# Performance work log

Hardware: AMD Instinct MI355X
Metric: run time of the kernel (lower is better)

The kernel has to match this reference:

```python
import jax, jax.numpy as jnp
import numpy as np

NHID = 1024
# Canonical DARTS recurrent genotype: (activation, predecessor-state index)
GENOTYPE = [("sigmoid", 0), ("relu", 1), ("relu", 1), ("identity", 1),
            ("tanh", 2), ("sigmoid", 5), ("tanh", 3), ("relu", 5)]
CONCAT = [1, 2, 3, 4, 5, 6, 7, 8]

_ACTS = {"tanh": jnp.tanh, "relu": jax.nn.relu,
         "sigmoid": jax.nn.sigmoid, "identity": lambda z: z}


def _cell(x, h_prev, W0, Ws):
    # x: [B, ninp], h_prev: [B, nhid]
    xh = jnp.concatenate([x, h_prev], axis=-1)              # [B, ninp+nhid]
    c0, h0 = jnp.split(xh @ W0, 2, axis=-1)                 # each [B, nhid]
    s0 = h_prev + jax.nn.sigmoid(c0) * (jnp.tanh(h0) - h_prev)
    states = [s0]
    for i, (name, pred) in enumerate(GENOTYPE):
        s_prev = states[pred]
        c, h = jnp.split(s_prev @ Ws[i], 2, axis=-1)
        s = s_prev + jax.nn.sigmoid(c) * (_ACTS[name](h) - s_prev)
        states.append(s)
    return jnp.mean(jnp.stack([states[i] for i in CONCAT], axis=-1), axis=-1)


def setup_inputs() -> dict:
    key = jax.random.key(0)
    k1, k2, k3 = jax.random.split(key, 3)
    T, B, NINP = 256, 256, 1024
    inputs = jax.random.normal(k1, (T, B, NINP), dtype=jnp.float32)
    h0 = jnp.zeros((B, NHID), dtype=jnp.float32)
    W0 = jax.random.normal(k2, (NINP + NHID, 2 * NHID), dtype=jnp.float32) * 0.02
    Ws = jax.random.normal(k3, (len(GENOTYPE), NHID, 2 * NHID), dtype=jnp.float32) * 0.02
    return {"inputs": inputs, "h0": h0, "W0": W0, "Ws": Ws}


def reference(inputs, h0, W0, Ws):
    def step(h, x):
        h_new = _cell(x, h, W0, Ws)
        return h_new, h_new
    _, hiddens = jax.lax.scan(step, h0, inputs)             # [T, B, nhid]
    return hiddens
```

## Files before the change

kernel.cpp:

```cpp
#include <hip/hip_runtime.h>


typedef short short8 __attribute__((ext_vector_type(8)));
typedef float floatx4 __attribute__((ext_vector_type(4)));

#define MFMA __builtin_amdgcn_mfma_f32_16x16x32_bf16

enum { ACT_SIG = 0, ACT_RELU = 1, ACT_TANH = 2, ACT_ID = 3 };

__device__ __forceinline__ unsigned short f2bf(float f) {
  unsigned u = __builtin_bit_cast(unsigned, f);
  u += 0x7fffu + ((u >> 16) & 1u);
  return (unsigned short)(u >> 16);
}

__device__ __forceinline__ float sigf(float z) { return 1.f / (1.f + __expf(-z)); }

__device__ __forceinline__ float actf(int a, float h) {
  if (a == ACT_SIG)  return sigf(h);
  if (a == ACT_RELU) return fmaxf(h, 0.f);
  if (a == ACT_TANH) return 1.f - 2.f / (__expf(2.f * h) + 1.f);
  return h;
}


struct GJob {
  const unsigned short* A;
  const unsigned short* Wt;
  const float* base;
  float* out_f;
  unsigned short* out_b;
  int act;
  int K;
};
struct GJobs { GJob j[3]; };

struct Set6 { short8 a0, a1, b0, b1, b2, b3; };

__device__ __forceinline__ void load6(Set6& s,
    const unsigned short* pa0, const unsigned short* pa1,
    const unsigned short* pb0, const unsigned short* pb1,
    const unsigned short* pb2, const unsigned short* pb3, int k) {
  s.a0 = *(const short8*)(pa0 + k);
  s.a1 = *(const short8*)(pa1 + k);
  s.b0 = *(const short8*)(pb0 + k);
  s.b1 = *(const short8*)(pb1 + k);
  s.b2 = *(const short8*)(pb2 + k);
  s.b3 = *(const short8*)(pb3 + k);
}

__device__ __forceinline__ void mm6(const Set6& s, floatx4 ac[2][2], floatx4 ah[2][2]) {
  ac[0][0] = MFMA(s.a0, s.b0, ac[0][0], 0, 0, 0);
  ac[1][0] = MFMA(s.a1, s.b0, ac[1][0], 0, 0, 0);
  ac[0][1] = MFMA(s.a0, s.b1, ac[0][1], 0, 0, 0);
  ac[1][1] = MFMA(s.a1, s.b1, ac[1][1], 0, 0, 0);
  ah[0][0] = MFMA(s.a0, s.b2, ah[0][0], 0, 0, 0);
  ah[1][0] = MFMA(s.a1, s.b2, ah[1][0], 0, 0, 0);
  ah[0][1] = MFMA(s.a0, s.b3, ah[0][1], 0, 0, 0);
  ah[1][1] = MFMA(s.a1, s.b3, ah[1][1], 0, 0, 0);
}

__global__ __launch_bounds__(256) void phase_gemm(GJobs jobs) {
  const GJob jb = jobs.j[blockIdx.z];
  const int K = jb.K;
  const int lane = threadIdx.x & 63;
  const int wave = threadIdx.x >> 6;
  const int col = lane & 15, quad = lane >> 4;
  const int m0  = blockIdx.y * 64 + (wave >> 1) * 32;
  const int sc0 = blockIdx.x * 64 + (wave & 1) * 32;

  const unsigned short* pa0 = jb.A + (size_t)(m0 + col) * K + quad * 8;
  const unsigned short* pa1 = pa0 + (size_t)16 * K;
  const unsigned short* pb0 = jb.Wt + (size_t)(sc0 + col) * K + quad * 8;
  const unsigned short* pb1 = pb0 + (size_t)16 * K;
  const unsigned short* pb2 = jb.Wt + (size_t)(1024 + sc0 + col) * K + quad * 8;
  const unsigned short* pb3 = pb2 + (size_t)16 * K;

  floatx4 ac[2][2], ah[2][2];
#pragma unroll
  for (int i = 0; i < 2; ++i)
#pragma unroll
    for (int j = 0; j < 2; ++j) {
      ac[i][j] = (floatx4){0.f, 0.f, 0.f, 0.f};
      ah[i][j] = (floatx4){0.f, 0.f, 0.f, 0.f};
    }

  Set6 s0, s1;
  load6(s0, pa0, pa1, pb0, pb1, pb2, pb3, 0);
  load6(s1, pa0, pa1, pb0, pb1, pb2, pb3, 32);
  for (int k = 64; k < K; k += 64) {
    mm6(s0, ac, ah);
    load6(s0, pa0, pa1, pb0, pb1, pb2, pb3, k);
    mm6(s1, ac, ah);
    load6(s1, pa0, pa1, pb0, pb1, pb2, pb3, k + 32);
  }
  mm6(s0, ac, ah);
  mm6(s1, ac, ah);

  const int act = jb.act;
#pragma unroll
  for (int mi = 0; mi < 2; ++mi)
#pragma unroll
    for (int ni = 0; ni < 2; ++ni)
#pragma unroll
      for (int rr = 0; rr < 4; ++rr) {
        int m = m0 + mi * 16 + quad * 4 + rr;
        int n = sc0 + ni * 16 + col;
        int idx = m * 1024 + n;
        float c = ac[mi][ni][rr];
        float h = ah[mi][ni][rr];
        float p = jb.base[idx];
        float v = fmaf(sigf(c), actf(act, h) - p, p);
        jb.out_f[idx] = v;
        if (jb.out_b) jb.out_b[idx] = f2bf(v);
      }
}

struct Set10 { short8 a0, a1, u0, u1, u2, u3, v0, v1, v2, v3; };

__global__ __launch_bounds__(256) void phase_e(
    const unsigned short* __restrict__ A,
    const unsigned short* __restrict__ W5t,
    const unsigned short* __restrict__ W7t,
    const float* __restrict__ m1, const float* __restrict__ m2,
    const float* __restrict__ m3, const float* __restrict__ m4,
    const float* __restrict__ m5, const float* __restrict__ m7,
    const float* __restrict__ xnext,
    float* __restrict__ out_t,
    unsigned short* __restrict__ xhb) {
  const int lane = threadIdx.x & 63;
  const int wave = threadIdx.x >> 6;
  const int col = lane & 15, quad = lane >> 4;
  const int m0  = blockIdx.y * 64 + (wave >> 1) * 32;
  const int sc0 = blockIdx.x * 64 + (wave & 1) * 32;
  const int K = 1024;

  const unsigned short* pa0 = A + (size_t)(m0 + col) * K + quad * 8;
  const unsigned short* pa1 = pa0 + (size_t)16 * K;
  const unsigned short* pu0 = W5t + (size_t)(sc0 + col) * K + quad * 8;
  const unsigned short* pu1 = pu0 + (size_t)16 * K;
  const unsigned short* pu2 = W5t + (size_t)(1024 + sc0 + col) * K + quad * 8;
  const unsigned short* pu3 = pu2 + (size_t)16 * K;
  const unsigned short* pv0 = W7t + (size_t)(sc0 + col) * K + quad * 8;
  const unsigned short* pv1 = pv0 + (size_t)16 * K;
  const unsigned short* pv2 = W7t + (size_t)(1024 + sc0 + col) * K + quad * 8;
  const unsigned short* pv3 = pv2 + (size_t)16 * K;

  floatx4 acc[4][2][2];
#pragma unroll
  for (int w = 0; w < 4; ++w)
#pragma unroll
    for (int i = 0; i < 2; ++i)
#pragma unroll
      for (int j = 0; j < 2; ++j) acc[w][i][j] = (floatx4){0.f, 0.f, 0.f, 0.f};

  Set10 s0, s1;
#define LOAD10(s, k)                                     \
  do {                                                   \
    s.a0 = *(const short8*)(pa0 + (k));                  \
    s.a1 = *(const short8*)(pa1 + (k));                  \
    s.u0 = *(const short8*)(pu0 + (k));                  \
    s.u1 = *(const short8*)(pu1 + (k));                  \
    s.u2 = *(const short8*)(pu2 + (k));                  \
    s.u3 = *(const short8*)(pu3 + (k));                  \
    s.v0 = *(const short8*)(pv0 + (k));                  \
    s.v1 = *(const short8*)(pv1 + (k));                  \
    s.v2 = *(const short8*)(pv2 + (k));                  \
    s.v3 = *(const short8*)(pv3 + (k));                  \
  } while (0)
#define MM10(s)                                          \
  do {                                                   \
    acc[0][0][0] = MFMA(s.a0, s.u0, acc[0][0][0], 0,0,0);\
    acc[0][1][0] = MFMA(s.a1, s.u0, acc[0][1][0], 0,0,0);\
    acc[0][0][1] = MFMA(s.a0, s.u1, acc[0][0][1], 0,0,0);\
    acc[0][1][1] = MFMA(s.a1, s.u1, acc[0][1][1], 0,0,0);\
    acc[1][0][0] = MFMA(s.a0, s.u2, acc[1][0][0], 0,0,0);\
    acc[1][1][0] = MFMA(s.a1, s.u2, acc[1][1][0], 0,0,0);\
    acc[1][0][1] = MFMA(s.a0, s.u3, acc[1][0][1], 0,0,0);\
    acc[1][1][1] = MFMA(s.a1, s.u3, acc[1][1][1], 0,0,0);\
    acc[2][0][0] = MFMA(s.a0, s.v0, acc[2][0][0], 0,0,0);\
    acc[2][1][0] = MFMA(s.a1, s.v0, acc[2][1][0], 0,0,0);\
    acc[2][0][1] = MFMA(s.a0, s.v1, acc[2][0][1], 0,0,0);\
    acc[2][1][1] = MFMA(s.a1, s.v1, acc[2][1][1], 0,0,0);\
    acc[3][0][0] = MFMA(s.a0, s.v2, acc[3][0][0], 0,0,0);\
    acc[3][1][0] = MFMA(s.a1, s.v2, acc[3][1][0], 0,0,0);\
    acc[3][0][1] = MFMA(s.a0, s.v3, acc[3][0][1], 0,0,0);\
    acc[3][1][1] = MFMA(s.a1, s.v3, acc[3][1][1], 0,0,0);\
  } while (0)

  LOAD10(s0, 0);
  LOAD10(s1, 32);
  for (int k = 64; k < K; k += 64) {
    MM10(s0);
    LOAD10(s0, k);
    MM10(s1);
    LOAD10(s1, k + 32);
  }
  MM10(s0);
  MM10(s1);

#pragma unroll
  for (int mi = 0; mi < 2; ++mi)
#pragma unroll
    for (int ni = 0; ni < 2; ++ni)
#pragma unroll
      for (int rr = 0; rr < 4; ++rr) {
        int m = m0 + mi * 16 + quad * 4 + rr;
        int n = sc0 + ni * 16 + col;
        int idx = m * 1024 + n;
        float b = m5[idx];
        float s6 = fmaf(sigf(acc[0][mi][ni][rr]), sigf(acc[1][mi][ni][rr]) - b, b);
        float s8 = fmaf(sigf(acc[2][mi][ni][rr]), fmaxf(acc[3][mi][ni][rr], 0.f) - b, b);
        float sum = m1[idx] + m2[idx] + m3[idx] + m4[idx] + b + m7[idx] + s6 + s8;
        float hh = sum * 0.125f;
        out_t[idx] = hh;
        xhb[m * 2048 + 1024 + n] = f2bf(hh);
        xhb[m * 2048 + n] = f2bf(xnext[idx]);
      }
}

__global__ __launch_bounds__(256) void conv_w(const float* __restrict__ W0,
                                              const float* __restrict__ Wsrc,
                                              unsigned short* __restrict__ wt) {
  int job = blockIdx.z;
  int K = (job == 0) ? 2048 : 1024;
  int kt = blockIdx.y;
  if (kt * 32 >= K) return;
  int nt = blockIdx.x;
  const float* W = (job == 0) ? W0 : (Wsrc + (size_t)(job - 1) * 1024 * 2048);
  unsigned short* Wt = (job == 0) ? wt
      : (wt + (size_t)2048 * 2048 + (size_t)(job - 1) * 2048 * 1024);

  __shared__ unsigned short tile[32][33];
  int tx = threadIdx.x & 31;
  int ty = threadIdx.x >> 5;
#pragma unroll
  for (int i = 0; i < 4; ++i) {
    int k = kt * 32 + ty + i * 8;
    tile[ty + i * 8][tx] = f2bf(W[(size_t)k * 2048 + nt * 32 + tx]);
  }
  __syncthreads();
#pragma unroll
  for (int i = 0; i < 4; ++i) {
    int n = nt * 32 + ty + i * 8;
    Wt[(size_t)n * K + kt * 32 + tx] = tile[tx][ty + i * 8];
  }
}

__global__ __launch_bounds__(256) void init_xh(const float* __restrict__ x0,
                                               const float* __restrict__ h0,
                                               unsigned short* __restrict__ xhb) {
  int i = blockIdx.x * 256 + threadIdx.x;
  int m = i >> 10, n = i & 1023;
  xhb[m * 2048 + n] = f2bf(x0[i]);
  xhb[m * 2048 + 1024 + n] = f2bf(h0[i]);
}

extern "C" void kernel_launch(void* const* d_in, const int* in_sizes, int n_in,
                              void* d_out, int out_size, void* d_ws, size_t ws_size,
                              hipStream_t stream) {
  const float* x_all = (const float*)d_in[0];
  const float* h0    = (const float*)d_in[1];
  const float* W0    = (const float*)d_in[2];
  const float* Ws    = (const float*)d_in[3];
  float* out = (float*)d_out;

  const size_t BH = (size_t)256 * 1024;

  unsigned short* wt0 = (unsigned short*)d_ws;
  unsigned short* wts[8];
  for (int i = 0; i < 8; ++i)
    wts[i] = wt0 + (size_t)2048 * 2048 + (size_t)i * 2048 * 1024;
  float* smbase = (float*)((char*)d_ws +
      (size_t)(2048 * 2048 + 8 * 2048 * 1024) * 2);
  float* sm[7];
  for (int i = 0; i < 7; ++i) sm[i] = smbase + (size_t)i * BH;
  unsigned short* sbbase = (unsigned short*)(smbase + (size_t)7 * BH);
  unsigned short* sb[5];
  for (int i = 0; i < 5; ++i) sb[i] = sbbase + (size_t)i * BH;
  unsigned short* xhb = sbbase + (size_t)5 * BH;

  conv_w<<<dim3(64, 64, 9), 256, 0, stream>>>(W0, Ws, wt0);
  init_xh<<<dim3(1024), 256, 0, stream>>>(x_all, h0, xhb);

  for (int t = 0; t < 256; ++t) {
    const float* hp = (t == 0) ? h0 : (out + (size_t)(t - 1) * BH);
    float* o_t = out + (size_t)t * BH;
    const float* xnext = x_all + (size_t)((t < 255) ? t + 1 : 255) * BH;

    GJobs J{};
    J.j[0] = { xhb, wt0, hp, sm[0], sb[0], ACT_TANH, 2048 };
    phase_gemm<<<dim3(16, 4, 1), 256, 0, stream>>>(J);

    J = GJobs{};
    J.j[0] = { sb[0], wts[0], sm[0], sm[1], sb[1], ACT_SIG, 1024 };
    phase_gemm<<<dim3(16, 4, 1), 256, 0, stream>>>(J);

    J = GJobs{};
    J.j[0] = { sb[1], wts[1], sm[1], sm[2], sb[2], ACT_RELU, 1024 };
    J.j[1] = { sb[1], wts[2], sm[1], sm[3], sb[3], ACT_RELU, 1024 };
    phase_gemm<<<dim3(16, 4, 2), 256, 0, stream>>>(J);

    J = GJobs{};
    J.j[0] = { sb[2], wts[4], sm[2], sm[5], sb[4], ACT_TANH, 1024 };
    J.j[1] = { sb[3], wts[6], sm[3], sm[6], nullptr, ACT_TANH, 1024 };
    J.j[2] = { sb[1], wts[3], sm[1], sm[4], nullptr, ACT_ID, 1024 };
    phase_gemm<<<dim3(16, 4, 3), 256, 0, stream>>>(J);

    phase_e<<<dim3(16, 4, 1), 256, 0, stream>>>(
        sb[4], wts[5], wts[7],
        sm[1], sm[2], sm[3], sm[4], sm[5], sm[6],
        xnext, o_t, xhb);
  }
}
```

Baseline: 44.52 ms.

## Replace per-step kernel launches with a persistent kernel using grid barriers

Replaces the 1280 small per-phase kernel launches with one persistent 256-block kernel that loops over timesteps and separates phases with an atomic-counter grid barrier. Tiles are made smaller (32x16 or 32x32 per wave) so 256 blocks, rather than 64-192, share each phase, and prefetch depth becomes a template parameter. The aim is to remove launch overhead and raise occupancy across CUs. In exchange it relies on every block being co-resident, and the spin barrier gives up after a timeout, which could silently yield wrong results.

```diff
diff --git a/kernel.cpp b/kernel.cpp
--- a/kernel.cpp
+++ b/kernel.cpp
@@ -23,200 +23,260 @@
   return h;
 }
 
-
-struct GJob {
-  const unsigned short* A;
-  const unsigned short* Wt;
-  const float* base;
-  float* out_f;
-  unsigned short* out_b;
-  int act;
-  int K;
-};
-struct GJobs { GJob j[3]; };
-
-struct Set6 { short8 a0, a1, b0, b1, b2, b3; };
-
-__device__ __forceinline__ void load6(Set6& s,
-    const unsigned short* pa0, const unsigned short* pa1,
-    const unsigned short* pb0, const unsigned short* pb1,
-    const unsigned short* pb2, const unsigned short* pb3, int k) {
-  s.a0 = *(const short8*)(pa0 + k);
-  s.a1 = *(const short8*)(pa1 + k);
-  s.b0 = *(const short8*)(pb0 + k);
-  s.b1 = *(const short8*)(pb1 + k);
-  s.b2 = *(const short8*)(pb2 + k);
-  s.b3 = *(const short8*)(pb3 + k);
-}
-
-__device__ __forceinline__ void mm6(const Set6& s, floatx4 ac[2][2], floatx4 ah[2][2]) {
-  ac[0][0] = MFMA(s.a0, s.b0, ac[0][0], 0, 0, 0);
-  ac[1][0] = MFMA(s.a1, s.b0, ac[1][0], 0, 0, 0);
-  ac[0][1] = MFMA(s.a0, s.b1, ac[0][1], 0, 0, 0);
-  ac[1][1] = MFMA(s.a1, s.b1, ac[1][1], 0, 0, 0);
-  ah[0][0] = MFMA(s.a0, s.b2, ah[0][0], 0, 0, 0);
-  ah[1][0] = MFMA(s.a1, s.b2, ah[1][0], 0, 0, 0);
-  ah[0][1] = MFMA(s.a0, s.b3, ah[0][1], 0, 0, 0);
-  ah[1][1] = MFMA(s.a1, s.b3, ah[1][1], 0, 0, 0);
-}
-
-__global__ __launch_bounds__(256) void phase_gemm(GJobs jobs) {
-  const GJob jb = jobs.j[blockIdx.z];
-  const int K = jb.K;
-  const int lane = threadIdx.x & 63;
-  const int wave = threadIdx.x >> 6;
+__device__ __forceinline__ bool grid_sync(unsigned* bar, unsigned target,
+                                          bool skip_wait) {
+  __shared__ int gs_flag;
+  __syncthreads();
+  if (threadIdx.x == 0) {
+    __hip_atomic_fetch_add(bar, 1u, __ATOMIC_RELEASE, __HIP_MEMORY_SCOPE_AGENT);
+    int ok = 1;
+    if (!skip_wait) {
+      int spins = 0;
+      while (__hip_atomic_load(bar, __ATOMIC_RELAXED,
+                               __HIP_MEMORY_SCOPE_AGENT) < target) {
+        __builtin_amdgcn_s_sleep(16);
+        if (++spins > (1 << 19)) { ok = 0; break; }
+      }
+    }
+    gs_flag = ok;
+  }
+  __syncthreads();
+  __builtin_amdgcn_fence(__ATOMIC_ACQUIRE, "agent");
+  return gs_flag != 0;
+}
+
+template <int NB, int DEPTH>
+__device__ __forceinline__ void g2_tile(
+    const unsigned short* __restrict__ A, const unsigned short* __restrict__ Wt,
+    const float* __restrict__ base, float* __restrict__ out_f,
+    unsigned short* __restrict__ out_b, int act, int K, int m0, int sc0,
+    int lane) {
   const int col = lane & 15, quad = lane >> 4;
-  const int m0  = blockIdx.y * 64 + (wave >> 1) * 32;
-  const int sc0 = blockIdx.x * 64 + (wave & 1) * 32;
-
-  const unsigned short* pa0 = jb.A + (size_t)(m0 + col) * K + quad * 8;
+  const unsigned short* pa0 = A + (size_t)(m0 + col) * K + quad * 8;
   const unsigned short* pa1 = pa0 + (size_t)16 * K;
-  const unsigned short* pb0 = jb.Wt + (size_t)(sc0 + col) * K + quad * 8;
-  const unsigned short* pb1 = pb0 + (size_t)16 * K;
-  const unsigned short* pb2 = jb.Wt + (size_t)(1024 + sc0 + col) * K + quad * 8;
-  const unsigned short* pb3 = pb2 + (size_t)16 * K;
-
-  floatx4 ac[2][2], ah[2][2];
+  const unsigned short* pbc[NB];
+  const unsigned short* pbh[NB];
+#pragma unroll
+  for (int j = 0; j < NB; ++j) {
+    pbc[j] = Wt + (size_t)(sc0 + 16 * j + col) * K + quad * 8;
+    pbh[j] = Wt + (size_t)(1024 + sc0 + 16 * j + col) * K + quad * 8;
+  }
+
+  floatx4 ac[2][NB], ah[2][NB];
 #pragma unroll
   for (int i = 0; i < 2; ++i)
 #pragma unroll
-    for (int j = 0; j < 2; ++j) {
+    for (int j = 0; j < NB; ++j) {
       ac[i][j] = (floatx4){0.f, 0.f, 0.f, 0.f};
       ah[i][j] = (floatx4){0.f, 0.f, 0.f, 0.f};
     }
 
-  Set6 s0, s1;
-  load6(s0, pa0, pa1, pb0, pb1, pb2, pb3, 0);
-  load6(s1, pa0, pa1, pb0, pb1, pb2, pb3, 32);
-  for (int k = 64; k < K; k += 64) {
-    mm6(s0, ac, ah);
-    load6(s0, pa0, pa1, pb0, pb1, pb2, pb3, k);
-    mm6(s1, ac, ah);
-    load6(s1, pa0, pa1, pb0, pb1, pb2, pb3, k + 32);
-  }
-  mm6(s0, ac, ah);
-  mm6(s1, ac, ah);
-
-  const int act = jb.act;
+  short8 ra0[DEPTH], ra1[DEPTH], rbc[DEPTH][NB], rbh[DEPTH][NB];
+
+#define G2_LD(s, k)                                                            \
+  {                                                                            \
+    ra0[s] = *(const short8*)(pa0 + (k));                                      \
+    ra1[s] = *(const short8*)(pa1 + (k));                                      \
+    _Pragma("unroll") for (int j = 0; j < NB; ++j) {                           \
+      rbc[s][j] = *(const short8*)(pbc[j] + (k));                              \
+      rbh[s][j] = *(const short8*)(pbh[j] + (k));                              \
+    }                                                                          \
+  }
+#define G2_MM(s)                                                               \
+  {                                                                            \
+    _Pragma("unroll") for (int j = 0; j < NB; ++j) {                           \
+      ac[0][j] = MFMA(ra0[s], rbc[s][j], ac[0][j], 0, 0, 0);                   \
+      ac[1][j] = MFMA(ra1[s], rbc[s][j], ac[1][j], 0, 0, 0);                   \
+      ah[0][j] = MFMA(ra0[s], rbh[s][j], ah[0][j], 0, 0, 0);                   \
+      ah[1][j] = MFMA(ra1[s], rbh[s][j], ah[1][j], 0, 0, 0);                   \
+    }                                                                          \
+  }
+
+#pragma unroll
+  for (int s = 0; s < DEPTH; ++s) G2_LD(s, s * 32);
+  for (int k = DEPTH * 32; k < K; k += DEPTH * 32) {
+#pragma unroll
+    for (int s = 0; s < DEPTH; ++s) {
+      G2_MM(s);
+      G2_LD(s, k + s * 32);
+    }
+  }
+#pragma unroll
+  for (int s = 0; s < DEPTH; ++s) G2_MM(s);
+#undef G2_LD
+#undef G2_MM
+
 #pragma unroll
   for (int mi = 0; mi < 2; ++mi)
 #pragma unroll
-    for (int ni = 0; ni < 2; ++ni)
+    for (int j = 0; j < NB; ++j)
 #pragma unroll
       for (int rr = 0; rr < 4; ++rr) {
         int m = m0 + mi * 16 + quad * 4 + rr;
-        int n = sc0 + ni * 16 + col;
+        int n = sc0 + j * 16 + col;
         int idx = m * 1024 + n;
-        float c = ac[mi][ni][rr];
-        float h = ah[mi][ni][rr];
-        float p = jb.base[idx];
+        float c = ac[mi][j][rr];
+        float h = ah[mi][j][rr];
+        float p = base[idx];
         float v = fmaf(sigf(c), actf(act, h) - p, p);
-        jb.out_f[idx] = v;
-        if (jb.out_b) jb.out_b[idx] = f2bf(v);
+        out_f[idx] = v;
+        if (out_b) out_b[idx] = f2bf(v);
       }
 }
 
-struct Set10 { short8 a0, a1, u0, u1, u2, u3, v0, v1, v2, v3; };
-
-__global__ __launch_bounds__(256) void phase_e(
-    const unsigned short* __restrict__ A,
-    const unsigned short* __restrict__ W5t,
-    const unsigned short* __restrict__ W7t,
-    const float* __restrict__ m1, const float* __restrict__ m2,
-    const float* __restrict__ m3, const float* __restrict__ m4,
-    const float* __restrict__ m5, const float* __restrict__ m7,
-    const float* __restrict__ xnext,
-    float* __restrict__ out_t,
-    unsigned short* __restrict__ xhb) {
-  const int lane = threadIdx.x & 63;
-  const int wave = threadIdx.x >> 6;
+__device__ __forceinline__ void e_tile(
+    const unsigned short* __restrict__ A, const unsigned short* __restrict__ W5t,
+    const unsigned short* __restrict__ W7t, const float* __restrict__ m1,
+    const float* __restrict__ m2, const float* __restrict__ m3,
+    const float* __restrict__ m4, const float* __restrict__ m5,
+    const float* __restrict__ m7, const float* __restrict__ xnext,
+    float* __restrict__ out_t, unsigned short* __restrict__ xhb,
+    int m0, int sc0, int lane) {
   const int col = lane & 15, quad = lane >> 4;
-  const int m0  = blockIdx.y * 64 + (wave >> 1) * 32;
-  const int sc0 = blockIdx.x * 64 + (wave & 1) * 32;
   const int K = 1024;
-
   const unsigned short* pa0 = A + (size_t)(m0 + col) * K + quad * 8;
   const unsigned short* pa1 = pa0 + (size_t)16 * K;
   const unsigned short* pu0 = W5t + (size_t)(sc0 + col) * K + quad * 8;
-  const unsigned short* pu1 = pu0 + (size_t)16 * K;
-  const unsigned short* pu2 = W5t + (size_t)(1024 + sc0 + col) * K + quad * 8;
-  const unsigned short* pu3 = pu2 + (size_t)16 * K;
+  const unsigned short* pu1 = W5t + (size_t)(1024 + sc0 + col) * K + quad * 8;
   const unsigned short* pv0 = W7t + (size_t)(sc0 + col) * K + quad * 8;
-  const unsigned short* pv1 = pv0 + (size_t)16 * K;
-  const unsigned short* pv2 = W7t + (size_t)(1024 + sc0 + col) * K + quad * 8;
-  const unsigned short* pv3 = pv2 + (size_t)16 * K;
-
-  floatx4 acc[4][2][2];
-#pragma unroll
-  for (int w = 0; w < 4; ++w)
-#pragma unroll
-    for (int i = 0; i < 2; ++i)
-#pragma unroll
-      for (int j = 0; j < 2; ++j) acc[w][i][j] = (floatx4){0.f, 0.f, 0.f, 0.f};
-
-  Set10 s0, s1;
-#define LOAD10(s, k)                                     \
-  do {                                                   \
-    s.a0 = *(const short8*)(pa0 + (k));                  \
-    s.a1 = *(const short8*)(pa1 + (k));                  \
-    s.u0 = *(const short8*)(pu0 + (k));                  \
-    s.u1 = *(const short8*)(pu1 + (k));                  \
-    s.u2 = *(const short8*)(pu2 + (k));                  \
-    s.u3 = *(const short8*)(pu3 + (k));                  \
-    s.v0 = *(const short8*)(pv0 + (k));                  \
-    s.v1 = *(const short8*)(pv1 + (k));                  \
-    s.v2 = *(const short8*)(pv2 + (k));                  \
-    s.v3 = *(const short8*)(pv3 + (k));                  \
-  } while (0)
-#define MM10(s)                                          \
-  do {                                                   \
-    acc[0][0][0] = MFMA(s.a0, s.u0, acc[0][0][0], 0,0,0);\
-    acc[0][1][0] = MFMA(s.a1, s.u0, acc[0][1][0], 0,0,0);\
-    acc[0][0][1] = MFMA(s.a0, s.u1, acc[0][0][1], 0,0,0);\
-    acc[0][1][1] = MFMA(s.a1, s.u1, acc[0][1][1], 0,0,0);\
-    acc[1][0][0] = MFMA(s.a0, s.u2, acc[1][0][0], 0,0,0);\
-    acc[1][1][0] = MFMA(s.a1, s.u2, acc[1][1][0], 0,0,0);\
-    acc[1][0][1] = MFMA(s.a0, s.u3, acc[1][0][1], 0,0,0);\
-    acc[1][1][1] = MFMA(s.a1, s.u3, acc[1][1][1], 0,0,0);\
-    acc[2][0][0] = MFMA(s.a0, s.v0, acc[2][0][0], 0,0,0);\
-    acc[2][1][0] = MFMA(s.a1, s.v0, acc[2][1][0], 0,0,0);\
-    acc[2][0][1] = MFMA(s.a0, s.v1, acc[2][0][1], 0,0,0);\
-    acc[2][1][1] = MFMA(s.a1, s.v1, acc[2][1][1], 0,0,0);\
-    acc[3][0][0] = MFMA(s.a0, s.v2, acc[3][0][0], 0,0,0);\
-    acc[3][1][0] = MFMA(s.a1, s.v2, acc[3][1][0], 0,0,0);\
-    acc[3][0][1] = MFMA(s.a0, s.v3, acc[3][0][1], 0,0,0);\
-    acc[3][1][1] = MFMA(s.a1, s.v3, acc[3][1][1], 0,0,0);\
-  } while (0)
-
-  LOAD10(s0, 0);
-  LOAD10(s1, 32);
+  const unsigned short* pv1 = W7t + (size_t)(1024 + sc0 + col) * K + quad * 8;
+
+  floatx4 c6[2], h6[2], c8[2], h8[2];
+#pragma unroll
+  for (int i = 0; i < 2; ++i) {
+    c6[i] = (floatx4){0.f, 0.f, 0.f, 0.f};
+    h6[i] = (floatx4){0.f, 0.f, 0.f, 0.f};
+    c8[i] = (floatx4){0.f, 0.f, 0.f, 0.f};
+    h8[i] = (floatx4){0.f, 0.f, 0.f, 0.f};
+  }
+
+  short8 ra0[2], ra1[2], ru0[2], ru1[2], rv0[2], rv1[2];
+#define E_LD(s, k)                              \
+  {                                             \
+    ra0[s] = *(const short8*)(pa0 + (k));       \
+    ra1[s] = *(const short8*)(pa1 + (k));       \
+    ru0[s] = *(const short8*)(pu0 + (k));       \
+    ru1[s] = *(const short8*)(pu1 + (k));       \
+    rv0[s] = *(const short8*)(pv0 + (k));       \
+    rv1[s] = *(const short8*)(pv1 + (k));       \
+  }
+#define E_MM(s)                                 \
+  {                                             \
+    c6[0] = MFMA(ra0[s], ru0[s], c6[0], 0, 0, 0); \
+    c6[1] = MFMA(ra1[s], ru0[s], c6[1], 0, 0, 0); \
+    h6[0] = MFMA(ra0[s], ru1[s], h6[0], 0, 0, 0); \
+    h6[1] = MFMA(ra1[s], ru1[s], h6[1], 0, 0, 0); \
+    c8[0] = MFMA(ra0[s], rv0[s], c8[0], 0, 0, 0); \
+    c8[1] = MFMA(ra1[s], rv0[s], c8[1], 0, 0, 0); \
+    h8[0] = MFMA(ra0[s], rv1[s], h8[0], 0, 0, 0); \
+    h8[1] = MFMA(ra1[s], rv1[s], h8[1], 0, 0, 0); \
+  }
+
+  E_LD(0, 0);
+  E_LD(1, 32);
   for (int k = 64; k < K; k += 64) {
-    MM10(s0);
-    LOAD10(s0, k);
-    MM10(s1);
-    LOAD10(s1, k + 32);
-  }
-  MM10(s0);
-  MM10(s1);
+    E_MM(0);
+    E_LD(0, k);
+    E_MM(1);
+    E_LD(1, k + 32);
+  }
+  E_MM(0);
+  E_MM(1);
+#undef E_LD
+#undef E_MM
 
 #pragma unroll
   for (int mi = 0; mi < 2; ++mi)
 #pragma unroll
-    for (int ni = 0; ni < 2; ++ni)
-#pragma unroll
-      for (int rr = 0; rr < 4; ++rr) {
-        int m = m0 + mi * 16 + quad * 4 + rr;
-        int n = sc0 + ni * 16 + col;
-        int idx = m * 1024 + n;
-        float b = m5[idx];
-        float s6 = fmaf(sigf(acc[0][mi][ni][rr]), sigf(acc[1][mi][ni][rr]) - b, b);
-        float s8 = fmaf(sigf(acc[2][mi][ni][rr]), fmaxf(acc[3][mi][ni][rr], 0.f) - b, b);
-        float sum = m1[idx] + m2[idx] + m3[idx] + m4[idx] + b + m7[idx] + s6 + s8;
-        float hh = sum * 0.125f;
-        out_t[idx] = hh;
-        xhb[m * 2048 + 1024 + n] = f2bf(hh);
-        xhb[m * 2048 + n] = f2bf(xnext[idx]);
-      }
+    for (int rr = 0; rr < 4; ++rr) {
+      int m = m0 + mi * 16 + quad * 4 + rr;
+      int n = sc0 + col;
+      int idx = m * 1024 + n;
+      float b = m5[idx];
+      float s6 = fmaf(sigf(c6[mi][rr]), sigf(h6[mi][rr]) - b, b);
+      float s8 = fmaf(sigf(c8[mi][rr]), fmaxf(h8[mi][rr], 0.f) - b, b);
+      float sum = m1[idx] + m2[idx] + m3[idx] + m4[idx] + b + m7[idx] + s6 + s8;
+      float hh = sum * 0.125f;
+      out_t[idx] = hh;
+      xhb[m * 2048 + 1024 + n] = f2bf(hh);
+      xhb[m * 2048 + n] = f2bf(xnext[idx]);
+    }
+}
+
+__global__ __launch_bounds__(512, 2) void darts_persist(
+    const float* __restrict__ x_all, const float* __restrict__ h0,
+    const unsigned short* __restrict__ wtb, float* out, float* __restrict__ smb,
+    unsigned short* __restrict__ sbb, unsigned short* __restrict__ xhb,
+    unsigned* __restrict__ bar) {
+  const size_t BH = (size_t)256 * 1024;
+  const int lane = threadIdx.x & 63;
+  const int wave = threadIdx.x >> 6;
+  const int blk = blockIdx.x;
+
+#define WTS(i) (wtb + (size_t)2048 * 2048 + (size_t)(i) * 2048 * 1024)
+  float* sm0 = smb;
+  float* sm1 = smb + 1 * BH;
+  float* sm2 = smb + 2 * BH;
+  float* sm3 = smb + 3 * BH;
+  float* sm4 = smb + 4 * BH;
+  float* sm5 = smb + 5 * BH;
+  float* sm6 = smb + 6 * BH;
+  unsigned short* sb0 = sbb;
+  unsigned short* sb1 = sbb + 1 * BH;
+  unsigned short* sb2 = sbb + 2 * BH;
+  unsigned short* sb3 = sbb + 3 * BH;
+  unsigned short* sb4 = sbb + 4 * BH;
+
+  bool poisoned = false;
+  unsigned tgt = 0;
+  for (int t = 0; t < 256; ++t) {
+    const float* hp = (t == 0) ? h0 : (out + (size_t)(t - 1) * BH);
+    float* o_t = out + (size_t)t * BH;
+    const float* xnext = x_all + (size_t)((t < 255) ? t + 1 : 255) * BH;
+
+    if (wave < 2) {
+      int tau = wave * 256 + blk;
+      g2_tile<1, 4>(xhb, wtb, hp, sm0, sb0, ACT_TANH, 2048,
+                    (tau >> 6) * 32, (tau & 63) * 16, lane);
+    }
+    tgt += 256; poisoned |= !grid_sync(bar, tgt, poisoned);
+
+    if (wave < 2) {
+      int tau = wave * 256 + blk;
+      g2_tile<1, 4>(sb0, WTS(0), sm0, sm1, sb1, ACT_SIG, 1024,
+                    (tau >> 6) * 32, (tau & 63) * 16, lane);
+    }
+    tgt += 256; poisoned |= !grid_sync(bar, tgt, poisoned);
+
+    if (wave < 3) {
+      const unsigned short* W = (wave == 0) ? WTS(1) : (wave == 1) ? WTS(2) : WTS(3);
+      float* of = (wave == 0) ? sm2 : (wave == 1) ? sm3 : sm4;
+      unsigned short* ob = (wave == 0) ? sb2 : (wave == 1) ? sb3 : (unsigned short*)nullptr;
+      int act = (wave == 2) ? ACT_ID : ACT_RELU;
+      g2_tile<2, 2>(sb1, W, sm1, of, ob, act, 1024,
+                    (blk >> 5) * 32, (blk & 31) * 32, lane);
+    }
+    tgt += 256; poisoned |= !grid_sync(bar, tgt, poisoned);
+
+    if (wave < 2) {
+      const unsigned short* Aop = (wave == 0) ? sb2 : sb3;
+      const unsigned short* W = (wave == 0) ? WTS(4) : WTS(6);
+      const float* bs = (wave == 0) ? sm2 : sm3;
+      float* of = (wave == 0) ? sm5 : sm6;
+      unsigned short* ob = (wave == 0) ? sb4 : (unsigned short*)nullptr;
+      g2_tile<2, 2>(Aop, W, bs, of, ob, ACT_TANH, 1024,
+                    (blk >> 5) * 32, (blk & 31) * 32, lane);
+    }
+    tgt += 256; poisoned |= !grid_sync(bar, tgt, poisoned);
+
+    if (wave < 2) {
+      int tau = wave * 256 + blk;
+      e_tile(sb4, WTS(5), WTS(7), sm1, sm2, sm3, sm4, sm5, sm6,
+             xnext, o_t, xhb, (tau >> 6) * 32, (tau & 63) * 16, lane);
+    }
+    tgt += 256; poisoned |= !grid_sync(bar, tgt, poisoned);
+  }
+#undef WTS
 }
 
 __global__ __launch_bounds__(256) void conv_w(const float* __restrict__ W0,
@@ -256,6 +316,8 @@
   xhb[m * 2048 + 1024 + n] = f2bf(h0[i]);
 }
 
+__global__ void zero_bar(unsigned* bar) { *bar = 0u; }
+
 extern "C" void kernel_launch(void* const* d_in, const int* in_sizes, int n_in,
                               void* d_out, int out_size, void* d_ws, size_t ws_size,
                               hipStream_t stream) {
@@ -268,48 +330,15 @@
   const size_t BH = (size_t)256 * 1024;
 
   unsigned short* wt0 = (unsigned short*)d_ws;
-  unsigned short* wts[8];
-  for (int i = 0; i < 8; ++i)
-    wts[i] = wt0 + (size_t)2048 * 2048 + (size_t)i * 2048 * 1024;
   float* smbase = (float*)((char*)d_ws +
       (size_t)(2048 * 2048 + 8 * 2048 * 1024) * 2);
-  float* sm[7];
-  for (int i = 0; i < 7; ++i) sm[i] = smbase + (size_t)i * BH;
   unsigned short* sbbase = (unsigned short*)(smbase + (size_t)7 * BH);
-  unsigned short* sb[5];
-  for (int i = 0; i < 5; ++i) sb[i] = sbbase + (size_t)i * BH;
   unsigned short* xhb = sbbase + (size_t)5 * BH;
+  unsigned* bar = (unsigned*)(xhb + (size_t)256 * 2048);
 
   conv_w<<<dim3(64, 64, 9), 256, 0, stream>>>(W0, Ws, wt0);
   init_xh<<<dim3(1024), 256, 0, stream>>>(x_all, h0, xhb);
-
-  for (int t = 0; t < 256; ++t) {
-    const float* hp = (t == 0) ? h0 : (out + (size_t)(t - 1) * BH);
-    float* o_t = out + (size_t)t * BH;
-    const float* xnext = x_all + (size_t)((t < 255) ? t + 1 : 255) * BH;
-
-    GJobs J{};
-    J.j[0] = { xhb, wt0, hp, sm[0], sb[0], ACT_TANH, 2048 };
-    phase_gemm<<<dim3(16, 4, 1), 256, 0, stream>>>(J);
-
-    J = GJobs{};
-    J.j[0] = { sb[0], wts[0], sm[0], sm[1], sb[1], ACT_SIG, 1024 };
-    phase_gemm<<<dim3(16, 4, 1), 256, 0, stream>>>(J);
-
-    J = GJobs{};
-    J.j[0] = { sb[1], wts[1], sm[1], sm[2], sb[2], ACT_RELU, 1024 };
-    J.j[1] = { sb[1], wts[2], sm[1], sm[3], sb[3], ACT_RELU, 1024 };
-    phase_gemm<<<dim3(16, 4, 2), 256, 0, stream>>>(J);
-
-    J = GJobs{};
-    J.j[0] = { sb[2], wts[4], sm[2], sm[5], sb[4], ACT_TANH, 1024 };
-    J.j[1] = { sb[3], wts[6], sm[3], sm[6], nullptr, ACT_TANH, 1024 };
-    J.j[2] = { sb[1], wts[3], sm[1], sm[4], nullptr, ACT_ID, 1024 };
-    phase_gemm<<<dim3(16, 4, 3), 256, 0, stream>>>(J);
-
-    phase_e<<<dim3(16, 4, 1), 256, 0, stream>>>(
-        sb[4], wts[5], wts[7],
-        sm[1], sm[2], sm[3], sm[4], sm[5], sm[6],
-        xnext, o_t, xhb);
-  }
-}
+  zero_bar<<<dim3(1), dim3(1), 0, stream>>>(bar);
+  darts_persist<<<dim3(256), dim3(512), 0, stream>>>(
+      x_all, h0, wt0, out, smbase, sbbase, xhb, bar);
+}
```

After: 70.61 ms. +58.6%, slower.
